# Performance work log

Hardware: AMD Instinct MI355X
Metric: run time of the kernel (lower is better)

## Reference

```python
import jax, jax.numpy as jnp
import numpy as np

B, S, H, P = 512, 256, 768, 32

def setup_inputs() -> dict:
    key = jax.random.key(0)
    k1, k2, k3, k4, k5, k6, k7, k8, k9 = jax.random.split(key, 9)
    physical_features_vec = jax.random.normal(k1, (B, S, H), dtype=jnp.float32)
    process_vec = jax.random.normal(k2, (B, S, H), dtype=jnp.float32)
    mirco_vec = jax.random.normal(k3, (B, S, H), dtype=jnp.float32)
    pos = jax.random.randint(k4, (B, P), 0, S, dtype=jnp.int64)
    # -1 padding (ragged lengths); keep column 0 always valid
    drop = jax.random.uniform(k5, (B, P)) < 0.3
    drop = drop.at[:, 0].set(False)
    alloy_pos = jnp.where(drop, jnp.int64(-1), pos)
    # Linear params (torch convention: W [out, in]), kaiming-uniform-ish init
    lim1 = 1.0 / np.sqrt(3 * H)
    W1 = jax.random.uniform(k6, (H, 3 * H), minval=-lim1, maxval=lim1, dtype=jnp.float32)
    b1 = jax.random.uniform(k7, (H,), minval=-lim1, maxval=lim1, dtype=jnp.float32)
    lim2 = 1.0 / np.sqrt(2 * H)
    W2 = jax.random.uniform(k8, (H, 2 * H), minval=-lim2, maxval=lim2, dtype=jnp.float32)
    b2 = jax.random.uniform(k9, (H,), minval=-lim2, maxval=lim2, dtype=jnp.float32)
    return {"physical_features_vec": physical_features_vec, "process_vec": process_vec,
            "mirco_vec": mirco_vec, "alloy_pos": alloy_pos,
            "W1": W1, "b1": b1, "W2": W2, "b2": b2}

def vec_pool(word_vec, pos):
    # masked gather + mean over valid positions (pos == -1 is padding)
    mask = pos != -1                                   # [B, P]
    safe = jnp.where(mask, pos, 0)                     # [B, P]
    gathered = jnp.take_along_axis(word_vec, safe[:, :, None], axis=1)  # [B, P, H]
    m = mask.astype(word_vec.dtype)[:, :, None]
    s = jnp.sum(gathered * m, axis=1)                  # [B, H]
    cnt = jnp.sum(m, axis=1)                           # [B, 1]
    return s / cnt

def l2norm(x, eps=1e-12):
    n = jnp.sqrt(jnp.sum(x * x, axis=1, keepdims=True))
    return x / jnp.maximum(n, eps)

def reference(physical_features_vec, process_vec, mirco_vec, alloy_pos, W1, b1, W2, b2):
    phys_sent = physical_features_vec[:, 0, :]
    pooled_proc = vec_pool(process_vec, alloy_pos)
    proc_sent = process_vec[:, 0, :]
    combined = jnp.concatenate([pooled_proc, proc_sent, phys_sent], axis=1)  # [B, 3H]
    combined = combined @ W1.T + b1
    normalized_combined = l2norm(combined)
    pooled_micro = vec_pool(mirco_vec, alloy_pos)
    micro_sent = mirco_vec[:, 0, :]
    micro = jnp.concatenate([pooled_micro, micro_sent], axis=1)  # [B, 2H]
    micro = micro @ W2.T + b2
    normalized_micro = l2norm(micro)
    return (normalized_combined, normalized_micro)
```

## Files before the change

### kernel.cpp

```cpp
#include <hip/hip_runtime.h>
#include <hip/hip_bf16.h>

#define B_  512
#define S_  256
#define H_  768
#define P_  32
#define K1_ 2304
#define K2_ 1536
#define N_  768
#define M_  512
#define NK1 72
#define NK2 48
#define CVT_BLOCKS 128

typedef __attribute__((ext_vector_type(8))) short bf16x8v;
typedef __attribute__((ext_vector_type(4))) float f32x4v;


__device__ inline unsigned short bfb(float x) {
  __hip_bfloat16 h = __float2bfloat16(x);
  return *reinterpret_cast<unsigned short*>(&h);
}

__device__ inline void store4_frag(__hip_bfloat16* __restrict__ buf, int NK,
                                   int m, int k, float4 v) {
  int m16 = m >> 4, mr = m & 15, k32 = k >> 5, kg = (k >> 3) & 3, e = k & 7;
  size_t off = ((size_t)(m16 * NK + k32) * 64 + kg * 16 + mr) * 8 + e;
  ushort4 u;
  u.x = bfb(v.x); u.y = bfb(v.y); u.z = bfb(v.z); u.w = bfb(v.w);
  *reinterpret_cast<ushort4*>(buf + off) = u;
}

__global__ __launch_bounds__(192) void pool_cvt_kernel(
    const float* __restrict__ phys, const float* __restrict__ proc,
    const float* __restrict__ micro, const int* __restrict__ pos,
    const float* __restrict__ W1, const float* __restrict__ W2,
    __hip_bfloat16* __restrict__ A1f, __hip_bfloat16* __restrict__ A2f,
    __hip_bfloat16* __restrict__ W1f, __hip_bfloat16* __restrict__ W2f) {
  const int t = threadIdx.x;
  const int NPOOL = 2 * B_;
  if (blockIdx.x < NPOOL) {
    const int b   = blockIdx.x >> 1;
    const int sel = blockIdx.x & 1;
    __shared__ int sp[P_];
    __shared__ int scnt;
    if (t < 64) {
      int p = (t < P_) ? pos[b * P_ + t] : -1;
      bool valid = (p != -1);
      unsigned long long m = __ballot(valid);
      int pre = __popcll(m & ((1ull << t) - 1ull));
      if (valid) sp[pre] = p;
      if (t == 0) scnt = (int)__popcll(m);
    }
    __syncthreads();
    const int c = scnt;
    const float inv = 1.0f / (float)c;

    const int H4 = H_ / 4;
    const float* base = (sel == 0) ? proc : micro;
    const float4* srcb = (const float4*)(base + (size_t)b * S_ * H_);

    float4 s = make_float4(0.f, 0.f, 0.f, 0.f);
    int i = 0;
    for (; i + 4 <= c; i += 4) {
      int p0 = sp[i], p1 = sp[i+1], p2 = sp[i+2], p3 = sp[i+3];
      float4 v0 = srcb[(size_t)p0 * H4 + t];
      float4 v1 = srcb[(size_t)p1 * H4 + t];
      float4 v2 = srcb[(size_t)p2 * H4 + t];
      float4 v3 = srcb[(size_t)p3 * H4 + t];
      s.x += v0.x + v1.x + v2.x + v3.x;
      s.y += v0.y + v1.y + v2.y + v3.y;
      s.z += v0.z + v1.z + v2.z + v3.z;
      s.w += v0.w + v1.w + v2.w + v3.w;
    }
    for (; i < c; ++i) {
      float4 v = srcb[(size_t)sp[i] * H4 + t];
      s.x += v.x; s.y += v.y; s.z += v.z; s.w += v.w;
    }
    float4 pooled = make_float4(s.x * inv, s.y * inv, s.z * inv, s.w * inv);
    float4 sent = srcb[t];

    const int k = t * 4;
    if (sel == 0) {
      store4_frag(A1f, NK1, b, k,          pooled);
      store4_frag(A1f, NK1, b, k + H_,     sent);
      float4 sph = ((const float4*)(phys + (size_t)b * S_ * H_))[t];
      store4_frag(A1f, NK1, b, k + 2*H_,   sph);
    } else {
      store4_frag(A2f, NK2, b, k,          pooled);
      store4_frag(A2f, NK2, b, k + H_,     sent);
    }
  } else {
    const int NG1 = 48 * NK1 * 64;
    const int NG2 = 48 * NK2 * 64;
    int tid = (blockIdx.x - NPOOL) * 192 + t;
    const int stride = CVT_BLOCKS * 192;
    for (int g = tid; g < NG1 + NG2; g += stride) {
      const float* W; __hip_bfloat16* Wf; int NK, K, gg;
      if (g < NG1) { W = W1; Wf = W1f; NK = NK1; K = K1_; gg = g; }
      else         { W = W2; Wf = W2f; NK = NK2; K = K2_; gg = g - NG1; }
      int lane = gg & 63;
      int rest = gg >> 6;
      int k32 = rest % NK;
      int n16 = rest / NK;
      int n = n16 * 16 + (lane & 15);
      int k = k32 * 32 + (lane >> 4) * 8;
      const float4* sW = (const float4*)(W + (size_t)n * K + k);
      float4 v0 = sW[0], v1 = sW[1];
      ushort4 u0, u1;
      u0.x = bfb(v0.x); u0.y = bfb(v0.y); u0.z = bfb(v0.z); u0.w = bfb(v0.w);
      u1.x = bfb(v1.x); u1.y = bfb(v1.y); u1.z = bfb(v1.z); u1.w = bfb(v1.w);
      ushort4* d = reinterpret_cast<ushort4*>(Wf + (size_t)gg * 8);
      d[0] = u0; d[1] = u1;
    }
  }
}

__global__ __launch_bounds__(64) void gemm_mfma_kernel(
    const __hip_bfloat16* __restrict__ A1f, const __hip_bfloat16* __restrict__ A2f,
    const __hip_bfloat16* __restrict__ W1f, const __hip_bfloat16* __restrict__ W2f,
    const float* __restrict__ b1, const float* __restrict__ b2,
    float* __restrict__ out) {
  int bid = blockIdx.x;
  const int TPG = (M_ / 32) * (N_ / 32);
  const __hip_bfloat16 *Af, *Wf;
  const float* bias; float* C; int NK;
  if (bid < TPG) { Af = A1f; Wf = W1f; bias = b1; C = out;                    NK = NK1; }
  else { bid -= TPG; Af = A2f; Wf = W2f; bias = b2; C = out + (size_t)M_*N_;  NK = NK2; }
  const int mt = bid / (N_ / 32);
  const int nt = bid % (N_ / 32);
  const int lane = threadIdx.x;

  const bf16x8v* A0 = (const bf16x8v*)Af + (size_t)(2 * mt) * NK * 64 + lane;
  const bf16x8v* A1 = A0 + (size_t)NK * 64;
  const bf16x8v* B0 = (const bf16x8v*)Wf + (size_t)(2 * nt) * NK * 64 + lane;
  const bf16x8v* B1 = B0 + (size_t)NK * 64;

  f32x4v acc00 = {0.f, 0.f, 0.f, 0.f};
  f32x4v acc01 = {0.f, 0.f, 0.f, 0.f};
  f32x4v acc10 = {0.f, 0.f, 0.f, 0.f};
  f32x4v acc11 = {0.f, 0.f, 0.f, 0.f};

#pragma unroll 4
  for (int k32 = 0; k32 < NK; ++k32) {
    bf16x8v a0 = A0[(size_t)k32 * 64];
    bf16x8v a1 = A1[(size_t)k32 * 64];
    bf16x8v w0 = B0[(size_t)k32 * 64];
    bf16x8v w1 = B1[(size_t)k32 * 64];
    acc00 = __builtin_amdgcn_mfma_f32_16x16x32_bf16(a0, w0, acc00, 0, 0, 0);
    acc01 = __builtin_amdgcn_mfma_f32_16x16x32_bf16(a0, w1, acc01, 0, 0, 0);
    acc10 = __builtin_amdgcn_mfma_f32_16x16x32_bf16(a1, w0, acc10, 0, 0, 0);
    acc11 = __builtin_amdgcn_mfma_f32_16x16x32_bf16(a1, w1, acc11, 0, 0, 0);
  }

  const int m0 = mt * 32, n0 = nt * 32;
  const int col = lane & 15;
  const int rg = (lane >> 4) * 4;
  const float bv0 = bias[n0 + col];
  const float bv1 = bias[n0 + 16 + col];
#pragma unroll
  for (int j = 0; j < 4; ++j) {
    const int r = rg + j;
    C[(size_t)(m0 + r) * N_ + n0 + col]           = acc00[j] + bv0;
    C[(size_t)(m0 + r) * N_ + n0 + 16 + col]      = acc01[j] + bv1;
    C[(size_t)(m0 + 16 + r) * N_ + n0 + col]      = acc10[j] + bv0;
    C[(size_t)(m0 + 16 + r) * N_ + n0 + 16 + col] = acc11[j] + bv1;
  }
}

__global__ __launch_bounds__(256) void norm_rows_kernel(float* __restrict__ out) {
  const int row = blockIdx.x;
  float* p = out + (size_t)row * N_;
  const int t = threadIdx.x;
  float x0 = p[t];
  float x1 = p[t + 256];
  float x2 = p[t + 512];
  float s = x0*x0 + x1*x1 + x2*x2;
#pragma unroll
  for (int off = 32; off > 0; off >>= 1) s += __shfl_down(s, off);
  __shared__ float ws[4];
  const int lane = t & 63, wid = t >> 6;
  if (lane == 0) ws[wid] = s;
  __syncthreads();
  float tot = ws[0] + ws[1] + ws[2] + ws[3];
  float inv = 1.0f / fmaxf(sqrtf(tot), 1e-12f);
  p[t]       = x0 * inv;
  p[t + 256] = x1 * inv;
  p[t + 512] = x2 * inv;
}

extern "C" void kernel_launch(void* const* d_in, const int* in_sizes, int n_in,
                              void* d_out, int out_size, void* d_ws, size_t ws_size,
                              hipStream_t stream) {
  const float* phys  = (const float*)d_in[0];
  const float* proc  = (const float*)d_in[1];
  const float* micro = (const float*)d_in[2];
  const int*   pos   = (const int*)d_in[3];
  const float* W1    = (const float*)d_in[4];
  const float* b1    = (const float*)d_in[5];
  const float* W2    = (const float*)d_in[6];
  const float* b2    = (const float*)d_in[7];
  float* out = (float*)d_out;

  __hip_bfloat16* A1f = (__hip_bfloat16*)d_ws;
  __hip_bfloat16* A2f = A1f + (size_t)32 * NK1 * 512;
  __hip_bfloat16* W1f = A2f + (size_t)32 * NK2 * 512;
  __hip_bfloat16* W2f = W1f + (size_t)48 * NK1 * 512;

  pool_cvt_kernel<<<2 * B_ + CVT_BLOCKS, 192, 0, stream>>>(
      phys, proc, micro, pos, W1, W2, A1f, A2f, W1f, W2f);
  gemm_mfma_kernel<<<2 * (M_ / 32) * (N_ / 32), 64, 0, stream>>>(
      A1f, A2f, W1f, W2f, b1, b2, out);
  norm_rows_kernel<<<2 * B_, 256, 0, stream>>>(out);
}
```

Measured before the change: 48.16 us.

## Fuse GEMM with row L2 normalization in one wide-block kernel

Replaces the separate bf16 MFMA GEMM and row-normalization kernels with one kernel. Each of 32 blocks of 12 waves computes a full 32-row by 768-column output tile, reduces row sums of squares through shuffles and shared memory, then writes already-normalized outputs. This removes a kernel launch and a read-modify-write pass over the output. The cost is a large drop in block count, so few CUs are busy and each block streams the whole weight matrix. The pooling loop is also unrolled to 8 gathers with two accumulators, and the sentence loads are hoisted ahead of it to raise memory-level parallelism.

After: 75.48 us. 1.57x slower.

```diff
diff --git a/kernel.cpp b/kernel.cpp
--- a/kernel.cpp
+++ b/kernel.cpp
@@ -60,31 +60,44 @@
     const float* base = (sel == 0) ? proc : micro;
     const float4* srcb = (const float4*)(base + (size_t)b * S_ * H_);
 
-    float4 s = make_float4(0.f, 0.f, 0.f, 0.f);
+    float4 sent = srcb[t];
+    float4 sph = make_float4(0.f, 0.f, 0.f, 0.f);
+    if (sel == 0) sph = ((const float4*)(phys + (size_t)b * S_ * H_))[t];
+
+    float4 s0 = make_float4(0.f, 0.f, 0.f, 0.f);
+    float4 s1 = make_float4(0.f, 0.f, 0.f, 0.f);
     int i = 0;
-    for (; i + 4 <= c; i += 4) {
-      int p0 = sp[i], p1 = sp[i+1], p2 = sp[i+2], p3 = sp[i+3];
-      float4 v0 = srcb[(size_t)p0 * H4 + t];
-      float4 v1 = srcb[(size_t)p1 * H4 + t];
-      float4 v2 = srcb[(size_t)p2 * H4 + t];
-      float4 v3 = srcb[(size_t)p3 * H4 + t];
-      s.x += v0.x + v1.x + v2.x + v3.x;
-      s.y += v0.y + v1.y + v2.y + v3.y;
-      s.z += v0.z + v1.z + v2.z + v3.z;
-      s.w += v0.w + v1.w + v2.w + v3.w;
-    }
-    for (; i < c; ++i) {
+    for (; i + 8 <= c; i += 8) {
+      float4 v0 = srcb[(size_t)sp[i+0] * H4 + t];
+      float4 v1 = srcb[(size_t)sp[i+1] * H4 + t];
+      float4 v2 = srcb[(size_t)sp[i+2] * H4 + t];
+      float4 v3 = srcb[(size_t)sp[i+3] * H4 + t];
+      float4 v4 = srcb[(size_t)sp[i+4] * H4 + t];
+      float4 v5 = srcb[(size_t)sp[i+5] * H4 + t];
+      float4 v6 = srcb[(size_t)sp[i+6] * H4 + t];
+      float4 v7 = srcb[(size_t)sp[i+7] * H4 + t];
+      s0.x += v0.x + v1.x + v2.x + v3.x;  s1.x += v4.x + v5.x + v6.x + v7.x;
+      s0.y += v0.y + v1.y + v2.y + v3.y;  s1.y += v4.y + v5.y + v6.y + v7.y;
+      s0.z += v0.z + v1.z + v2.z + v3.z;  s1.z += v4.z + v5.z + v6.z + v7.z;
+      s0.w += v0.w + v1.w + v2.w + v3.w;  s1.w += v4.w + v5.w + v6.w + v7.w;
+    }
+    for (; i + 2 <= c; i += 2) {
+      float4 v0 = srcb[(size_t)sp[i+0] * H4 + t];
+      float4 v1 = srcb[(size_t)sp[i+1] * H4 + t];
+      s0.x += v0.x + v1.x; s0.y += v0.y + v1.y;
+      s0.z += v0.z + v1.z; s0.w += v0.w + v1.w;
+    }
+    if (i < c) {
       float4 v = srcb[(size_t)sp[i] * H4 + t];
-      s.x += v.x; s.y += v.y; s.z += v.z; s.w += v.w;
-    }
-    float4 pooled = make_float4(s.x * inv, s.y * inv, s.z * inv, s.w * inv);
-    float4 sent = srcb[t];
+      s0.x += v.x; s0.y += v.y; s0.z += v.z; s0.w += v.w;
+    }
+    float4 pooled = make_float4((s0.x + s1.x) * inv, (s0.y + s1.y) * inv,
+                                (s0.z + s1.z) * inv, (s0.w + s1.w) * inv);
 
     const int k = t * 4;
     if (sel == 0) {
       store4_frag(A1f, NK1, b, k,          pooled);
       store4_frag(A1f, NK1, b, k + H_,     sent);
-      float4 sph = ((const float4*)(phys + (size_t)b * S_ * H_))[t];
       store4_frag(A1f, NK1, b, k + 2*H_,   sph);
     } else {
       store4_frag(A2f, NK2, b, k,          pooled);
@@ -116,77 +129,121 @@
   }
 }
 
-__global__ __launch_bounds__(64) void gemm_mfma_kernel(
+__device__ inline f32x4v shfl_xor4(f32x4v v, int m) {
+  f32x4v r;
+  r[0] = __shfl_xor(v[0], m);
+  r[1] = __shfl_xor(v[1], m);
+  r[2] = __shfl_xor(v[2], m);
+  r[3] = __shfl_xor(v[3], m);
+  return r;
+}
+
+template <int NK>
+__device__ inline void gemm_norm_body(const bf16x8v* __restrict__ Af,
+                                      const bf16x8v* __restrict__ Wf,
+                                      const float* __restrict__ bias,
+                                      float* __restrict__ C, int mt) {
+  const int tid = threadIdx.x;
+  const int w = tid >> 6;
+  const int lane = tid & 63;
+  const int col = lane & 15;
+  const int rg = (lane >> 4) * 4;
+  const int n0w = w * 64;
+
+  const bf16x8v* A0 = Af + (size_t)(2 * mt) * NK * 64 + lane;
+  const bf16x8v* A1 = A0 + (size_t)NK * 64;
+  const bf16x8v* B0 = Wf + (size_t)(4 * w) * NK * 64 + lane;
+
+  f32x4v acc[2][4];
+#pragma unroll
+  for (int i = 0; i < 2; ++i)
+#pragma unroll
+    for (int j = 0; j < 4; ++j) acc[i][j] = (f32x4v){0.f, 0.f, 0.f, 0.f};
+
+#pragma unroll 2
+  for (int k = 0; k < NK; ++k) {
+    bf16x8v a0 = A0[(size_t)k * 64];
+    bf16x8v a1 = A1[(size_t)k * 64];
+    bf16x8v w0 = B0[(size_t)k * 64];
+    bf16x8v w1 = B0[(size_t)k * 64 + (size_t)NK * 64];
+    bf16x8v w2 = B0[(size_t)k * 64 + (size_t)2 * NK * 64];
+    bf16x8v w3 = B0[(size_t)k * 64 + (size_t)3 * NK * 64];
+    acc[0][0] = __builtin_amdgcn_mfma_f32_16x16x32_bf16(a0, w0, acc[0][0], 0, 0, 0);
+    acc[0][1] = __builtin_amdgcn_mfma_f32_16x16x32_bf16(a0, w1, acc[0][1], 0, 0, 0);
+    acc[0][2] = __builtin_amdgcn_mfma_f32_16x16x32_bf16(a0, w2, acc[0][2], 0, 0, 0);
+    acc[0][3] = __builtin_amdgcn_mfma_f32_16x16x32_bf16(a0, w3, acc[0][3], 0, 0, 0);
+    acc[1][0] = __builtin_amdgcn_mfma_f32_16x16x32_bf16(a1, w0, acc[1][0], 0, 0, 0);
+    acc[1][1] = __builtin_amdgcn_mfma_f32_16x16x32_bf16(a1, w1, acc[1][1], 0, 0, 0);
+    acc[1][2] = __builtin_amdgcn_mfma_f32_16x16x32_bf16(a1, w2, acc[1][2], 0, 0, 0);
+    acc[1][3] = __builtin_amdgcn_mfma_f32_16x16x32_bf16(a1, w3, acc[1][3], 0, 0, 0);
+  }
+
+#pragma unroll
+  for (int j = 0; j < 4; ++j) {
+    float bj = bias[n0w + j * 16 + col];
+#pragma unroll
+    for (int e = 0; e < 4; ++e) { acc[0][j][e] += bj; acc[1][j][e] += bj; }
+  }
+
+  f32x4v q0 = (f32x4v){0.f, 0.f, 0.f, 0.f};
+  f32x4v q1 = (f32x4v){0.f, 0.f, 0.f, 0.f};
+#pragma unroll
+  for (int j = 0; j < 4; ++j)
+#pragma unroll
+    for (int e = 0; e < 4; ++e) {
+      q0[e] += acc[0][j][e] * acc[0][j][e];
+      q1[e] += acc[1][j][e] * acc[1][j][e];
+    }
+#pragma unroll
+  for (int m = 1; m < 16; m <<= 1) {
+    f32x4v t0 = shfl_xor4(q0, m), t1 = shfl_xor4(q1, m);
+#pragma unroll
+    for (int e = 0; e < 4; ++e) { q0[e] += t0[e]; q1[e] += t1[e]; }
+  }
+
+  __shared__ float partials[12][32];
+  __shared__ float sinv[32];
+  if (col == 0) {
+#pragma unroll
+    for (int e = 0; e < 4; ++e) {
+      partials[w][rg + e]      = q0[e];
+      partials[w][16 + rg + e] = q1[e];
+    }
+  }
+  __syncthreads();
+  if (tid < 32) {
+    float s = 0.f;
+#pragma unroll
+    for (int ww = 0; ww < 12; ++ww) s += partials[ww][tid];
+    sinv[tid] = 1.0f / fmaxf(sqrtf(s), 1e-12f);
+  }
+  __syncthreads();
+
+  const int m0 = mt * 32;
+#pragma unroll
+  for (int e = 0; e < 4; ++e) {
+    float i0 = sinv[rg + e];
+    float i1 = sinv[16 + rg + e];
+#pragma unroll
+    for (int j = 0; j < 4; ++j) {
+      C[(size_t)(m0 + rg + e) * N_ + n0w + j * 16 + col]      = acc[0][j][e] * i0;
+      C[(size_t)(m0 + 16 + rg + e) * N_ + n0w + j * 16 + col] = acc[1][j][e] * i1;
+    }
+  }
+}
+
+__global__ __launch_bounds__(768) void gemm_norm_kernel(
     const __hip_bfloat16* __restrict__ A1f, const __hip_bfloat16* __restrict__ A2f,
     const __hip_bfloat16* __restrict__ W1f, const __hip_bfloat16* __restrict__ W2f,
     const float* __restrict__ b1, const float* __restrict__ b2,
     float* __restrict__ out) {
-  int bid = blockIdx.x;
-  const int TPG = (M_ / 32) * (N_ / 32);
-  const __hip_bfloat16 *Af, *Wf;
-  const float* bias; float* C; int NK;
-  if (bid < TPG) { Af = A1f; Wf = W1f; bias = b1; C = out;                    NK = NK1; }
-  else { bid -= TPG; Af = A2f; Wf = W2f; bias = b2; C = out + (size_t)M_*N_;  NK = NK2; }
-  const int mt = bid / (N_ / 32);
-  const int nt = bid % (N_ / 32);
-  const int lane = threadIdx.x;
-
-  const bf16x8v* A0 = (const bf16x8v*)Af + (size_t)(2 * mt) * NK * 64 + lane;
-  const bf16x8v* A1 = A0 + (size_t)NK * 64;
-  const bf16x8v* B0 = (const bf16x8v*)Wf + (size_t)(2 * nt) * NK * 64 + lane;
-  const bf16x8v* B1 = B0 + (size_t)NK * 64;
-
-  f32x4v acc00 = {0.f, 0.f, 0.f, 0.f};
-  f32x4v acc01 = {0.f, 0.f, 0.f, 0.f};
-  f32x4v acc10 = {0.f, 0.f, 0.f, 0.f};
-  f32x4v acc11 = {0.f, 0.f, 0.f, 0.f};
-
-#pragma unroll 4
-  for (int k32 = 0; k32 < NK; ++k32) {
-    bf16x8v a0 = A0[(size_t)k32 * 64];
-    bf16x8v a1 = A1[(size_t)k32 * 64];
-    bf16x8v w0 = B0[(size_t)k32 * 64];
-    bf16x8v w1 = B1[(size_t)k32 * 64];
-    acc00 = __builtin_amdgcn_mfma_f32_16x16x32_bf16(a0, w0, acc00, 0, 0, 0);
-    acc01 = __builtin_amdgcn_mfma_f32_16x16x32_bf16(a0, w1, acc01, 0, 0, 0);
-    acc10 = __builtin_amdgcn_mfma_f32_16x16x32_bf16(a1, w0, acc10, 0, 0, 0);
-    acc11 = __builtin_amdgcn_mfma_f32_16x16x32_bf16(a1, w1, acc11, 0, 0, 0);
-  }
-
-  const int m0 = mt * 32, n0 = nt * 32;
-  const int col = lane & 15;
-  const int rg = (lane >> 4) * 4;
-  const float bv0 = bias[n0 + col];
-  const float bv1 = bias[n0 + 16 + col];
-#pragma unroll
-  for (int j = 0; j < 4; ++j) {
-    const int r = rg + j;
-    C[(size_t)(m0 + r) * N_ + n0 + col]           = acc00[j] + bv0;
-    C[(size_t)(m0 + r) * N_ + n0 + 16 + col]      = acc01[j] + bv1;
-    C[(size_t)(m0 + 16 + r) * N_ + n0 + col]      = acc10[j] + bv0;
-    C[(size_t)(m0 + 16 + r) * N_ + n0 + 16 + col] = acc11[j] + bv1;
-  }
-}
-
-__global__ __launch_bounds__(256) void norm_rows_kernel(float* __restrict__ out) {
-  const int row = blockIdx.x;
-  float* p = out + (size_t)row * N_;
-  const int t = threadIdx.x;
-  float x0 = p[t];
-  float x1 = p[t + 256];
-  float x2 = p[t + 512];
-  float s = x0*x0 + x1*x1 + x2*x2;
-#pragma unroll
-  for (int off = 32; off > 0; off >>= 1) s += __shfl_down(s, off);
-  __shared__ float ws[4];
-  const int lane = t & 63, wid = t >> 6;
-  if (lane == 0) ws[wid] = s;
-  __syncthreads();
-  float tot = ws[0] + ws[1] + ws[2] + ws[3];
-  float inv = 1.0f / fmaxf(sqrtf(tot), 1e-12f);
-  p[t]       = x0 * inv;
-  p[t + 256] = x1 * inv;
-  p[t + 512] = x2 * inv;
+  const int bid = blockIdx.x;
+  if (bid < 16) {
+    gemm_norm_body<NK1>((const bf16x8v*)A1f, (const bf16x8v*)W1f, b1, out, bid);
+  } else {
+    gemm_norm_body<NK2>((const bf16x8v*)A2f, (const bf16x8v*)W2f, b2,
+                        out + (size_t)M_ * N_, bid - 16);
+  }
 }
 
 extern "C" void kernel_launch(void* const* d_in, const int* in_sizes, int n_in,
@@ -209,7 +266,5 @@
 
   pool_cvt_kernel<<<2 * B_ + CVT_BLOCKS, 192, 0, stream>>>(
       phys, proc, micro, pos, W1, W2, A1f, A2f, W1f, W2f);
-  gemm_mfma_kernel<<<2 * (M_ / 32) * (N_ / 32), 64, 0, stream>>>(
-      A1f, A2f, W1f, W2f, b1, b2, out);
-  norm_rows_kernel<<<2 * B_, 256, 0, stream>>>(out);
-}
+  gemm_norm_kernel<<<32, 768, 0, stream>>>(A1f, A2f, W1f, W2f, b1, b2, out);
+}
```

## Use 64x64 GEMM tiles on row-major bf16 operands with XCD-aware block mapping

Applied to the files above, without the earlier changes.

The GEMM moves from 32x32 tiles (768 single-wave blocks) to 64x64 tiles computed by one wave with a 4x4 MFMA accumulator grid over 192 blocks. Block IDs are remapped so tiles sharing A and W rows land on the same XCD for better L2 reuse. Activations and weights are now stored row-major in bf16 instead of the pre-swizzled fragment layout. The pooling loop is unrolled to 8 gathers with two accumulators, and the sentence loads are hoisted ahead of it. The risks are low parallelism (192 waves), high register pressure from 64 accumulator floats per lane, and strided fragment loads from the row-major layout.

Measured after the change: 76.99 us. +59.9%, slower.

```diff
diff --git a/kernel.cpp b/kernel.cpp
--- a/kernel.cpp
+++ b/kernel.cpp
@@ -9,34 +9,23 @@
 #define K2_ 1536
 #define N_  768
 #define M_  512
-#define NK1 72
-#define NK2 48
 #define CVT_BLOCKS 128
 
 typedef __attribute__((ext_vector_type(8))) short bf16x8v;
+typedef __attribute__((ext_vector_type(8))) unsigned short u16x8;
 typedef __attribute__((ext_vector_type(4))) float f32x4v;
-
 
 __device__ inline unsigned short bfb(float x) {
   __hip_bfloat16 h = __float2bfloat16(x);
   return *reinterpret_cast<unsigned short*>(&h);
-}
-
-__device__ inline void store4_frag(__hip_bfloat16* __restrict__ buf, int NK,
-                                   int m, int k, float4 v) {
-  int m16 = m >> 4, mr = m & 15, k32 = k >> 5, kg = (k >> 3) & 3, e = k & 7;
-  size_t off = ((size_t)(m16 * NK + k32) * 64 + kg * 16 + mr) * 8 + e;
-  ushort4 u;
-  u.x = bfb(v.x); u.y = bfb(v.y); u.z = bfb(v.z); u.w = bfb(v.w);
-  *reinterpret_cast<ushort4*>(buf + off) = u;
 }
 
 __global__ __launch_bounds__(192) void pool_cvt_kernel(
     const float* __restrict__ phys, const float* __restrict__ proc,
     const float* __restrict__ micro, const int* __restrict__ pos,
     const float* __restrict__ W1, const float* __restrict__ W2,
-    __hip_bfloat16* __restrict__ A1f, __hip_bfloat16* __restrict__ A2f,
-    __hip_bfloat16* __restrict__ W1f, __hip_bfloat16* __restrict__ W2f) {
+    __hip_bfloat16* __restrict__ Ab1, __hip_bfloat16* __restrict__ Ab2,
+    __hip_bfloat16* __restrict__ Wb1, __hip_bfloat16* __restrict__ Wb2) {
   const int t = threadIdx.x;
   const int NPOOL = 2 * B_;
   if (blockIdx.x < NPOOL) {
@@ -60,111 +49,138 @@
     const float* base = (sel == 0) ? proc : micro;
     const float4* srcb = (const float4*)(base + (size_t)b * S_ * H_);
 
-    float4 s = make_float4(0.f, 0.f, 0.f, 0.f);
+    float4 sent = srcb[t];
+    float4 sph = make_float4(0.f, 0.f, 0.f, 0.f);
+    if (sel == 0) sph = ((const float4*)(phys + (size_t)b * S_ * H_))[t];
+
+    float4 s0 = make_float4(0.f, 0.f, 0.f, 0.f);
+    float4 s1 = make_float4(0.f, 0.f, 0.f, 0.f);
     int i = 0;
-    for (; i + 4 <= c; i += 4) {
-      int p0 = sp[i], p1 = sp[i+1], p2 = sp[i+2], p3 = sp[i+3];
-      float4 v0 = srcb[(size_t)p0 * H4 + t];
-      float4 v1 = srcb[(size_t)p1 * H4 + t];
-      float4 v2 = srcb[(size_t)p2 * H4 + t];
-      float4 v3 = srcb[(size_t)p3 * H4 + t];
-      s.x += v0.x + v1.x + v2.x + v3.x;
-      s.y += v0.y + v1.y + v2.y + v3.y;
-      s.z += v0.z + v1.z + v2.z + v3.z;
-      s.w += v0.w + v1.w + v2.w + v3.w;
-    }
-    for (; i < c; ++i) {
+    for (; i + 8 <= c; i += 8) {
+      float4 v0 = srcb[(size_t)sp[i+0] * H4 + t];
+      float4 v1 = srcb[(size_t)sp[i+1] * H4 + t];
+      float4 v2 = srcb[(size_t)sp[i+2] * H4 + t];
+      float4 v3 = srcb[(size_t)sp[i+3] * H4 + t];
+      float4 v4 = srcb[(size_t)sp[i+4] * H4 + t];
+      float4 v5 = srcb[(size_t)sp[i+5] * H4 + t];
+      float4 v6 = srcb[(size_t)sp[i+6] * H4 + t];
+      float4 v7 = srcb[(size_t)sp[i+7] * H4 + t];
+      s0.x += v0.x + v1.x + v2.x + v3.x;  s1.x += v4.x + v5.x + v6.x + v7.x;
+      s0.y += v0.y + v1.y + v2.y + v3.y;  s1.y += v4.y + v5.y + v6.y + v7.y;
+      s0.z += v0.z + v1.z + v2.z + v3.z;  s1.z += v4.z + v5.z + v6.z + v7.z;
+      s0.w += v0.w + v1.w + v2.w + v3.w;  s1.w += v4.w + v5.w + v6.w + v7.w;
+    }
+    for (; i + 2 <= c; i += 2) {
+      float4 v0 = srcb[(size_t)sp[i+0] * H4 + t];
+      float4 v1 = srcb[(size_t)sp[i+1] * H4 + t];
+      s0.x += v0.x + v1.x; s0.y += v0.y + v1.y;
+      s0.z += v0.z + v1.z; s0.w += v0.w + v1.w;
+    }
+    if (i < c) {
       float4 v = srcb[(size_t)sp[i] * H4 + t];
-      s.x += v.x; s.y += v.y; s.z += v.z; s.w += v.w;
-    }
-    float4 pooled = make_float4(s.x * inv, s.y * inv, s.z * inv, s.w * inv);
-    float4 sent = srcb[t];
-
-    const int k = t * 4;
+      s0.x += v.x; s0.y += v.y; s0.z += v.z; s0.w += v.w;
+    }
+    float4 pooled = make_float4((s0.x + s1.x) * inv, (s0.y + s1.y) * inv,
+                                (s0.z + s1.z) * inv, (s0.w + s1.w) * inv);
+
+    ushort4 up, us;
+    up.x = bfb(pooled.x); up.y = bfb(pooled.y); up.z = bfb(pooled.z); up.w = bfb(pooled.w);
+    us.x = bfb(sent.x);   us.y = bfb(sent.y);   us.z = bfb(sent.z);   us.w = bfb(sent.w);
     if (sel == 0) {
-      store4_frag(A1f, NK1, b, k,          pooled);
-      store4_frag(A1f, NK1, b, k + H_,     sent);
-      float4 sph = ((const float4*)(phys + (size_t)b * S_ * H_))[t];
-      store4_frag(A1f, NK1, b, k + 2*H_,   sph);
+      __hip_bfloat16* row = Ab1 + (size_t)b * K1_;
+      *reinterpret_cast<ushort4*>(row + t*4)          = up;
+      *reinterpret_cast<ushort4*>(row + H_ + t*4)     = us;
+      ushort4 uh;
+      uh.x = bfb(sph.x); uh.y = bfb(sph.y); uh.z = bfb(sph.z); uh.w = bfb(sph.w);
+      *reinterpret_cast<ushort4*>(row + 2*H_ + t*4)   = uh;
     } else {
-      store4_frag(A2f, NK2, b, k,          pooled);
-      store4_frag(A2f, NK2, b, k + H_,     sent);
+      __hip_bfloat16* row = Ab2 + (size_t)b * K2_;
+      *reinterpret_cast<ushort4*>(row + t*4)          = up;
+      *reinterpret_cast<ushort4*>(row + H_ + t*4)     = us;
     }
   } else {
-    const int NG1 = 48 * NK1 * 64;
-    const int NG2 = 48 * NK2 * 64;
+    const int G1 = (768 * K1_) / 8;
+    const int G2 = (768 * K2_) / 8;
     int tid = (blockIdx.x - NPOOL) * 192 + t;
     const int stride = CVT_BLOCKS * 192;
-    for (int g = tid; g < NG1 + NG2; g += stride) {
-      const float* W; __hip_bfloat16* Wf; int NK, K, gg;
-      if (g < NG1) { W = W1; Wf = W1f; NK = NK1; K = K1_; gg = g; }
-      else         { W = W2; Wf = W2f; NK = NK2; K = K2_; gg = g - NG1; }
-      int lane = gg & 63;
-      int rest = gg >> 6;
-      int k32 = rest % NK;
-      int n16 = rest / NK;
-      int n = n16 * 16 + (lane & 15);
-      int k = k32 * 32 + (lane >> 4) * 8;
-      const float4* sW = (const float4*)(W + (size_t)n * K + k);
-      float4 v0 = sW[0], v1 = sW[1];
-      ushort4 u0, u1;
-      u0.x = bfb(v0.x); u0.y = bfb(v0.y); u0.z = bfb(v0.z); u0.w = bfb(v0.w);
-      u1.x = bfb(v1.x); u1.y = bfb(v1.y); u1.z = bfb(v1.z); u1.w = bfb(v1.w);
-      ushort4* d = reinterpret_cast<ushort4*>(Wf + (size_t)gg * 8);
-      d[0] = u0; d[1] = u1;
+    for (int g = tid; g < G1 + G2; g += stride) {
+      const float* src; __hip_bfloat16* dst; int gg;
+      if (g < G1) { src = W1; dst = Wb1; gg = g; }
+      else        { src = W2; dst = Wb2; gg = g - G1; }
+      const float4* s = (const float4*)(src + (size_t)gg * 8);
+      float4 v0 = s[0], v1 = s[1];
+      u16x8 o;
+      o[0] = bfb(v0.x); o[1] = bfb(v0.y); o[2] = bfb(v0.z); o[3] = bfb(v0.w);
+      o[4] = bfb(v1.x); o[5] = bfb(v1.y); o[6] = bfb(v1.z); o[7] = bfb(v1.w);
+      *reinterpret_cast<u16x8*>(dst + (size_t)gg * 8) = o;
     }
   }
 }
 
-__global__ __launch_bounds__(64) void gemm_mfma_kernel(
-    const __hip_bfloat16* __restrict__ A1f, const __hip_bfloat16* __restrict__ A2f,
-    const __hip_bfloat16* __restrict__ W1f, const __hip_bfloat16* __restrict__ W2f,
+template <int K>
+__device__ inline void gemm_body(const __hip_bfloat16* __restrict__ Ab,
+                                 const __hip_bfloat16* __restrict__ Wb,
+                                 const float* __restrict__ bias,
+                                 float* __restrict__ C, int mt, int nt) {
+  const int lane = threadIdx.x;
+  const int col16 = lane & 15;
+  const int kg = lane >> 2 >> 2;
+  const int m0 = mt * 64, n0 = nt * 64;
+
+  const __hip_bfloat16* pA = Ab + (size_t)(m0 + col16) * K + kg * 8;
+  const __hip_bfloat16* pW = Wb + (size_t)(n0 + col16) * K + kg * 8;
+
+  f32x4v acc[4][4];
+#pragma unroll
+  for (int a = 0; a < 4; ++a)
+#pragma unroll
+    for (int b = 0; b < 4; ++b) acc[a][b] = (f32x4v){0.f, 0.f, 0.f, 0.f};
+
+#pragma unroll 2
+  for (int k32 = 0; k32 < K / 32; ++k32) {
+    bf16x8v af[4], wf[4];
+#pragma unroll
+    for (int i = 0; i < 4; ++i) {
+      af[i] = *(const bf16x8v*)(pA + (size_t)i * 16 * K + k32 * 32);
+      wf[i] = *(const bf16x8v*)(pW + (size_t)i * 16 * K + k32 * 32);
+    }
+#pragma unroll
+    for (int a = 0; a < 4; ++a)
+#pragma unroll
+      for (int b = 0; b < 4; ++b)
+        acc[a][b] = __builtin_amdgcn_mfma_f32_16x16x32_bf16(af[a], wf[b], acc[a][b], 0, 0, 0);
+  }
+
+  const int rg = (lane >> 4) * 4;
+  float bv[4];
+#pragma unroll
+  for (int b = 0; b < 4; ++b) bv[b] = bias[n0 + b * 16 + col16];
+#pragma unroll
+  for (int a = 0; a < 4; ++a)
+#pragma unroll
+    for (int j = 0; j < 4; ++j) {
+      float* crow = C + (size_t)(m0 + a * 16 + rg + j) * N_ + n0 + col16;
+#pragma unroll
+      for (int b = 0; b < 4; ++b) crow[b * 16] = acc[a][b][j] + bv[b];
+    }
+}
+
+__global__ __launch_bounds__(64) void gemm_kernel(
+    const __hip_bfloat16* __restrict__ Ab1, const __hip_bfloat16* __restrict__ Ab2,
+    const __hip_bfloat16* __restrict__ Wb1, const __hip_bfloat16* __restrict__ Wb2,
     const float* __restrict__ b1, const float* __restrict__ b2,
     float* __restrict__ out) {
-  int bid = blockIdx.x;
-  const int TPG = (M_ / 32) * (N_ / 32);
-  const __hip_bfloat16 *Af, *Wf;
-  const float* bias; float* C; int NK;
-  if (bid < TPG) { Af = A1f; Wf = W1f; bias = b1; C = out;                    NK = NK1; }
-  else { bid -= TPG; Af = A2f; Wf = W2f; bias = b2; C = out + (size_t)M_*N_;  NK = NK2; }
-  const int mt = bid / (N_ / 32);
-  const int nt = bid % (N_ / 32);
-  const int lane = threadIdx.x;
-
-  const bf16x8v* A0 = (const bf16x8v*)Af + (size_t)(2 * mt) * NK * 64 + lane;
-  const bf16x8v* A1 = A0 + (size_t)NK * 64;
-  const bf16x8v* B0 = (const bf16x8v*)Wf + (size_t)(2 * nt) * NK * 64 + lane;
-  const bf16x8v* B1 = B0 + (size_t)NK * 64;
-
-  f32x4v acc00 = {0.f, 0.f, 0.f, 0.f};
-  f32x4v acc01 = {0.f, 0.f, 0.f, 0.f};
-  f32x4v acc10 = {0.f, 0.f, 0.f, 0.f};
-  f32x4v acc11 = {0.f, 0.f, 0.f, 0.f};
-
-#pragma unroll 4
-  for (int k32 = 0; k32 < NK; ++k32) {
-    bf16x8v a0 = A0[(size_t)k32 * 64];
-    bf16x8v a1 = A1[(size_t)k32 * 64];
-    bf16x8v w0 = B0[(size_t)k32 * 64];
-    bf16x8v w1 = B1[(size_t)k32 * 64];
-    acc00 = __builtin_amdgcn_mfma_f32_16x16x32_bf16(a0, w0, acc00, 0, 0, 0);
-    acc01 = __builtin_amdgcn_mfma_f32_16x16x32_bf16(a0, w1, acc01, 0, 0, 0);
-    acc10 = __builtin_amdgcn_mfma_f32_16x16x32_bf16(a1, w0, acc10, 0, 0, 0);
-    acc11 = __builtin_amdgcn_mfma_f32_16x16x32_bf16(a1, w1, acc11, 0, 0, 0);
-  }
-
-  const int m0 = mt * 32, n0 = nt * 32;
-  const int col = lane & 15;
-  const int rg = (lane >> 4) * 4;
-  const float bv0 = bias[n0 + col];
-  const float bv1 = bias[n0 + 16 + col];
-#pragma unroll
-  for (int j = 0; j < 4; ++j) {
-    const int r = rg + j;
-    C[(size_t)(m0 + r) * N_ + n0 + col]           = acc00[j] + bv0;
-    C[(size_t)(m0 + r) * N_ + n0 + 16 + col]      = acc01[j] + bv1;
-    C[(size_t)(m0 + 16 + r) * N_ + n0 + col]      = acc10[j] + bv0;
-    C[(size_t)(m0 + 16 + r) * N_ + n0 + 16 + col] = acc11[j] + bv1;
+  const int orig = blockIdx.x;
+  const int xcd = orig & 7;
+  const int slot = orig >> 3;
+  const int g = xcd >> 2;
+  const int x = xcd & 3;
+  const int mt = (x >> 1) * 4 + slot / 6;
+  const int nt = (x & 1) * 6 + slot % 6;
+  if (g == 0) {
+    gemm_body<K1_>(Ab1, Wb1, b1, out, mt, nt);
+  } else {
+    gemm_body<K2_>(Ab2, Wb2, b2, out + (size_t)M_ * N_, mt, nt);
   }
 }
 
@@ -202,14 +218,13 @@
   const float* b2    = (const float*)d_in[7];
   float* out = (float*)d_out;
 
-  __hip_bfloat16* A1f = (__hip_bfloat16*)d_ws;
-  __hip_bfloat16* A2f = A1f + (size_t)32 * NK1 * 512;
-  __hip_bfloat16* W1f = A2f + (size_t)32 * NK2 * 512;
-  __hip_bfloat16* W2f = W1f + (size_t)48 * NK1 * 512;
+  __hip_bfloat16* Ab1 = (__hip_bfloat16*)d_ws;
+  __hip_bfloat16* Ab2 = Ab1 + (size_t)M_ * K1_;
+  __hip_bfloat16* Wb1 = Ab2 + (size_t)M_ * K2_;
+  __hip_bfloat16* Wb2 = Wb1 + (size_t)N_ * K1_;
 
   pool_cvt_kernel<<<2 * B_ + CVT_BLOCKS, 192, 0, stream>>>(
-      phys, proc, micro, pos, W1, W2, A1f, A2f, W1f, W2f);
-  gemm_mfma_kernel<<<2 * (M_ / 32) * (N_ / 32), 64, 0, stream>>>(
-      A1f, A2f, W1f, W2f, b1, b2, out);
+      phys, proc, micro, pos, W1, W2, Ab1, Ab2, Wb1, Wb2);
+  gemm_kernel<<<192, 64, 0, stream>>>(Ab1, Ab2, Wb1, Wb2, b1, b2, out);
   norm_rows_kernel<<<2 * B_, 256, 0, stream>>>(out);
 }
```

## Remap block indices for XCD locality, software-pipeline GEMM loads, deepen pooling unroll

Applied to the files above, without the earlier changes.

The pooling blocks are remapped so that blocks landing on the same XCD (bid&7) write adjacent 16-row fragment groups. The GEMM block mapping is changed so that each XCD handles a fixed group of N tiles, which improves L2 reuse of the weight fragments. The GEMM loop is templated on NK and double-buffered, so loads for the next two k-steps are issued before the current MFMAs run. The pooling gather is unrolled to 8 loads with two accumulators, the sentence row is loaded before the gather, and the weight conversion uses a single 16-byte store. Register pressure goes up in exchange.

After: 48.18 us. Within noise of the previous version (+0.0%).

```diff
diff --git a/kernel.cpp b/kernel.cpp
--- a/kernel.cpp
+++ b/kernel.cpp
@@ -14,13 +14,14 @@
 #define CVT_BLOCKS 128
 
 typedef __attribute__((ext_vector_type(8))) short bf16x8v;
+typedef __attribute__((ext_vector_type(8))) unsigned short u16x8;
 typedef __attribute__((ext_vector_type(4))) float f32x4v;
-
 
 __device__ inline unsigned short bfb(float x) {
   __hip_bfloat16 h = __float2bfloat16(x);
   return *reinterpret_cast<unsigned short*>(&h);
 }
+
 
 __device__ inline void store4_frag(__hip_bfloat16* __restrict__ buf, int NK,
                                    int m, int k, float4 v) {
@@ -40,8 +41,18 @@
   const int t = threadIdx.x;
   const int NPOOL = 2 * B_;
   if (blockIdx.x < NPOOL) {
-    const int b   = blockIdx.x >> 1;
-    const int sel = blockIdx.x & 1;
+    const int bid = blockIdx.x;
+    const int x = bid & 7;
+    const int r2 = bid >> 3;
+    const int e = r2 & 3;
+    const int sghi = r2 >> 2;
+    const int sg = sghi * 8 + x;
+    const int rsub = sg & 3;
+    const int selm = sg >> 2;
+    const int sel = selm >> 5;
+    const int m16 = selm & 31;
+    const int b = m16 * 16 + rsub * 4 + e;
+
     __shared__ int sp[P_];
     __shared__ int scnt;
     if (t < 64) {
@@ -60,31 +71,44 @@
     const float* base = (sel == 0) ? proc : micro;
     const float4* srcb = (const float4*)(base + (size_t)b * S_ * H_);
 
-    float4 s = make_float4(0.f, 0.f, 0.f, 0.f);
+    float4 sent = srcb[t];
+    float4 sph = make_float4(0.f, 0.f, 0.f, 0.f);
+    if (sel == 0) sph = ((const float4*)(phys + (size_t)b * S_ * H_))[t];
+
+    float4 s0 = make_float4(0.f, 0.f, 0.f, 0.f);
+    float4 s1 = make_float4(0.f, 0.f, 0.f, 0.f);
     int i = 0;
-    for (; i + 4 <= c; i += 4) {
-      int p0 = sp[i], p1 = sp[i+1], p2 = sp[i+2], p3 = sp[i+3];
-      float4 v0 = srcb[(size_t)p0 * H4 + t];
-      float4 v1 = srcb[(size_t)p1 * H4 + t];
-      float4 v2 = srcb[(size_t)p2 * H4 + t];
-      float4 v3 = srcb[(size_t)p3 * H4 + t];
-      s.x += v0.x + v1.x + v2.x + v3.x;
-      s.y += v0.y + v1.y + v2.y + v3.y;
-      s.z += v0.z + v1.z + v2.z + v3.z;
-      s.w += v0.w + v1.w + v2.w + v3.w;
-    }
-    for (; i < c; ++i) {
+    for (; i + 8 <= c; i += 8) {
+      float4 v0 = srcb[(size_t)sp[i+0] * H4 + t];
+      float4 v1 = srcb[(size_t)sp[i+1] * H4 + t];
+      float4 v2 = srcb[(size_t)sp[i+2] * H4 + t];
+      float4 v3 = srcb[(size_t)sp[i+3] * H4 + t];
+      float4 v4 = srcb[(size_t)sp[i+4] * H4 + t];
+      float4 v5 = srcb[(size_t)sp[i+5] * H4 + t];
+      float4 v6 = srcb[(size_t)sp[i+6] * H4 + t];
+      float4 v7 = srcb[(size_t)sp[i+7] * H4 + t];
+      s0.x += v0.x + v1.x + v2.x + v3.x;  s1.x += v4.x + v5.x + v6.x + v7.x;
+      s0.y += v0.y + v1.y + v2.y + v3.y;  s1.y += v4.y + v5.y + v6.y + v7.y;
+      s0.z += v0.z + v1.z + v2.z + v3.z;  s1.z += v4.z + v5.z + v6.z + v7.z;
+      s0.w += v0.w + v1.w + v2.w + v3.w;  s1.w += v4.w + v5.w + v6.w + v7.w;
+    }
+    for (; i + 2 <= c; i += 2) {
+      float4 v0 = srcb[(size_t)sp[i+0] * H4 + t];
+      float4 v1 = srcb[(size_t)sp[i+1] * H4 + t];
+      s0.x += v0.x + v1.x; s0.y += v0.y + v1.y;
+      s0.z += v0.z + v1.z; s0.w += v0.w + v1.w;
+    }
+    if (i < c) {
       float4 v = srcb[(size_t)sp[i] * H4 + t];
-      s.x += v.x; s.y += v.y; s.z += v.z; s.w += v.w;
-    }
-    float4 pooled = make_float4(s.x * inv, s.y * inv, s.z * inv, s.w * inv);
-    float4 sent = srcb[t];
+      s0.x += v.x; s0.y += v.y; s0.z += v.z; s0.w += v.w;
+    }
+    float4 pooled = make_float4((s0.x + s1.x) * inv, (s0.y + s1.y) * inv,
+                                (s0.z + s1.z) * inv, (s0.w + s1.w) * inv);
 
     const int k = t * 4;
     if (sel == 0) {
       store4_frag(A1f, NK1, b, k,          pooled);
       store4_frag(A1f, NK1, b, k + H_,     sent);
-      float4 sph = ((const float4*)(phys + (size_t)b * S_ * H_))[t];
       store4_frag(A1f, NK1, b, k + 2*H_,   sph);
     } else {
       store4_frag(A2f, NK2, b, k,          pooled);
@@ -107,33 +131,30 @@
       int k = k32 * 32 + (lane >> 4) * 8;
       const float4* sW = (const float4*)(W + (size_t)n * K + k);
       float4 v0 = sW[0], v1 = sW[1];
-      ushort4 u0, u1;
-      u0.x = bfb(v0.x); u0.y = bfb(v0.y); u0.z = bfb(v0.z); u0.w = bfb(v0.w);
-      u1.x = bfb(v1.x); u1.y = bfb(v1.y); u1.z = bfb(v1.z); u1.w = bfb(v1.w);
-      ushort4* d = reinterpret_cast<ushort4*>(Wf + (size_t)gg * 8);
-      d[0] = u0; d[1] = u1;
-    }
-  }
-}
-
-__global__ __launch_bounds__(64) void gemm_mfma_kernel(
-    const __hip_bfloat16* __restrict__ A1f, const __hip_bfloat16* __restrict__ A2f,
-    const __hip_bfloat16* __restrict__ W1f, const __hip_bfloat16* __restrict__ W2f,
-    const float* __restrict__ b1, const float* __restrict__ b2,
-    float* __restrict__ out) {
-  int bid = blockIdx.x;
-  const int TPG = (M_ / 32) * (N_ / 32);
-  const __hip_bfloat16 *Af, *Wf;
-  const float* bias; float* C; int NK;
-  if (bid < TPG) { Af = A1f; Wf = W1f; bias = b1; C = out;                    NK = NK1; }
-  else { bid -= TPG; Af = A2f; Wf = W2f; bias = b2; C = out + (size_t)M_*N_;  NK = NK2; }
-  const int mt = bid / (N_ / 32);
-  const int nt = bid % (N_ / 32);
+      u16x8 o;
+      o[0] = bfb(v0.x); o[1] = bfb(v0.y); o[2] = bfb(v0.z); o[3] = bfb(v0.w);
+      o[4] = bfb(v1.x); o[5] = bfb(v1.y); o[6] = bfb(v1.z); o[7] = bfb(v1.w);
+      *reinterpret_cast<u16x8*>(Wf + (size_t)gg * 8) = o;
+    }
+  }
+}
+
+#define MFMA4(A0V, A1V, W0V, W1V)                                             \
+  acc00 = __builtin_amdgcn_mfma_f32_16x16x32_bf16(A0V, W0V, acc00, 0, 0, 0);  \
+  acc01 = __builtin_amdgcn_mfma_f32_16x16x32_bf16(A0V, W1V, acc01, 0, 0, 0);  \
+  acc10 = __builtin_amdgcn_mfma_f32_16x16x32_bf16(A1V, W0V, acc10, 0, 0, 0);  \
+  acc11 = __builtin_amdgcn_mfma_f32_16x16x32_bf16(A1V, W1V, acc11, 0, 0, 0);
+
+template <int NK>
+__device__ inline void gemm_body(const bf16x8v* __restrict__ Af,
+                                 const bf16x8v* __restrict__ Wf,
+                                 const float* __restrict__ bias,
+                                 float* __restrict__ C, int mt, int nt) {
   const int lane = threadIdx.x;
 
-  const bf16x8v* A0 = (const bf16x8v*)Af + (size_t)(2 * mt) * NK * 64 + lane;
+  const bf16x8v* A0 = Af + (size_t)(2 * mt) * NK * 64 + lane;
   const bf16x8v* A1 = A0 + (size_t)NK * 64;
-  const bf16x8v* B0 = (const bf16x8v*)Wf + (size_t)(2 * nt) * NK * 64 + lane;
+  const bf16x8v* B0 = Wf + (size_t)(2 * nt) * NK * 64 + lane;
   const bf16x8v* B1 = B0 + (size_t)NK * 64;
 
   f32x4v acc00 = {0.f, 0.f, 0.f, 0.f};
@@ -141,17 +162,25 @@
   f32x4v acc10 = {0.f, 0.f, 0.f, 0.f};
   f32x4v acc11 = {0.f, 0.f, 0.f, 0.f};
 
-#pragma unroll 4
-  for (int k32 = 0; k32 < NK; ++k32) {
-    bf16x8v a0 = A0[(size_t)k32 * 64];
-    bf16x8v a1 = A1[(size_t)k32 * 64];
-    bf16x8v w0 = B0[(size_t)k32 * 64];
-    bf16x8v w1 = B1[(size_t)k32 * 64];
-    acc00 = __builtin_amdgcn_mfma_f32_16x16x32_bf16(a0, w0, acc00, 0, 0, 0);
-    acc01 = __builtin_amdgcn_mfma_f32_16x16x32_bf16(a0, w1, acc01, 0, 0, 0);
-    acc10 = __builtin_amdgcn_mfma_f32_16x16x32_bf16(a1, w0, acc10, 0, 0, 0);
-    acc11 = __builtin_amdgcn_mfma_f32_16x16x32_bf16(a1, w1, acc11, 0, 0, 0);
-  }
+  bf16x8v a0s0 = A0[0],  a1s0 = A1[0],  w0s0 = B0[0],  w1s0 = B1[0];
+  bf16x8v a0s1 = A0[64], a1s1 = A1[64], w0s1 = B0[64], w1s1 = B1[64];
+
+  for (int k = 0; k < NK - 2; k += 2) {
+    bf16x8v pa0 = A0[(size_t)(k + 2) * 64];
+    bf16x8v pa1 = A1[(size_t)(k + 2) * 64];
+    bf16x8v pw0 = B0[(size_t)(k + 2) * 64];
+    bf16x8v pw1 = B1[(size_t)(k + 2) * 64];
+    bf16x8v qa0 = A0[(size_t)(k + 3) * 64];
+    bf16x8v qa1 = A1[(size_t)(k + 3) * 64];
+    bf16x8v qw0 = B0[(size_t)(k + 3) * 64];
+    bf16x8v qw1 = B1[(size_t)(k + 3) * 64];
+    MFMA4(a0s0, a1s0, w0s0, w1s0)
+    MFMA4(a0s1, a1s1, w0s1, w1s1)
+    a0s0 = pa0; a1s0 = pa1; w0s0 = pw0; w1s0 = pw1;
+    a0s1 = qa0; a1s1 = qa1; w0s1 = qw0; w1s1 = qw1;
+  }
+  MFMA4(a0s0, a1s0, w0s0, w1s0)
+  MFMA4(a0s1, a1s1, w0s1, w1s1)
 
   const int m0 = mt * 32, n0 = nt * 32;
   const int col = lane & 15;
@@ -165,6 +194,24 @@
     C[(size_t)(m0 + r) * N_ + n0 + 16 + col]      = acc01[j] + bv1;
     C[(size_t)(m0 + 16 + r) * N_ + n0 + col]      = acc10[j] + bv0;
     C[(size_t)(m0 + 16 + r) * N_ + n0 + 16 + col] = acc11[j] + bv1;
+  }
+}
+
+__global__ __launch_bounds__(64) void gemm_mfma_kernel(
+    const __hip_bfloat16* __restrict__ A1f, const __hip_bfloat16* __restrict__ A2f,
+    const __hip_bfloat16* __restrict__ W1f, const __hip_bfloat16* __restrict__ W2f,
+    const float* __restrict__ b1, const float* __restrict__ b2,
+    float* __restrict__ out) {
+  const int bid = blockIdx.x;
+  const int x = bid & 7;
+  const int local = bid >> 3;
+  const int mt = local / 6;
+  const int ntp = x * 6 + local % 6;
+  if (ntp < 24) {
+    gemm_body<NK1>((const bf16x8v*)A1f, (const bf16x8v*)W1f, b1, out, mt, ntp);
+  } else {
+    gemm_body<NK2>((const bf16x8v*)A2f, (const bf16x8v*)W2f, b2,
+                   out + (size_t)M_ * N_, mt, ntp - 24);
   }
 }
 
```
